# Optimization experiments

Hardware: AMD Instinct MI355X
Metric: run time of the kernel (lower is better)

Reference implementation:

```python
import jax, jax.numpy as jnp
import numpy as np

THRESHOLD = 0.02  # matches init threshold
N_POINTS = 4_000_000
N_PLANES = 64


def setup_inputs() -> dict:
    key = jax.random.key(0)
    k1, k2, k3 = jax.random.split(key, 3)
    points = jax.random.uniform(k1, (N_POINTS, 3), dtype=jnp.float32)
    normals = jax.random.normal(k2, (N_PLANES, 3), dtype=jnp.float32)
    normals = normals / jnp.linalg.norm(normals, axis=1, keepdims=True)
    # anchor each plane at a random point inside the cube so it intersects the cloud
    anchors = jax.random.uniform(k3, (N_PLANES, 3), dtype=jnp.float32)
    distances = jnp.sum(normals * anchors, axis=1)
    return {"points": points, "normals": normals, "distances": distances}


def reference(points, normals, distances):
    """Sequential per-plane SVD refinement + masked projection (faithful to torch loop).

    Plane fits (mask, centroid, covariance) use the ORIGINAL points, as in the
    source; only the projection is applied cumulatively to the running state.
    """
    dtype = points.dtype
    jitter = jnp.diag(jnp.asarray([1.0, 2.0, 3.0], dtype))  # keeps eigh well-posed for invalid planes

    def step(proj, plane):
        n, d = plane
        # inlier mask on original points (data-dependent in torch; here a weight vector)
        m = (jnp.abs(points @ n - d) < THRESHOLD).astype(dtype)  # (N,)
        cnt = jnp.sum(m)
        validf = (cnt >= 3.0).astype(dtype)
        centroid = jnp.sum(m[:, None] * points, axis=0) / jnp.maximum(cnt, 1.0)  # (3,)
        xc = (points - centroid) * m[:, None]  # masked centered points (N,3)
        cov = xc.T @ xc  # (3,3), m is 0/1 so single weighting == mask-select
        cov = cov + (1.0 - validf) * jitter
        # smallest-eigenvalue eigenvector of symmetric cov == torch V[:, 2] (up to sign)
        _, V = jnp.linalg.eigh(cov)
        rn = V[:, 0]
        rn = jnp.where(jnp.dot(rn, n) < 0.0, -rn, rn)  # align with coarse normal
        rd = jnp.dot(centroid, rn)
        # project only masked points of the running state onto refined plane
        delta = (proj @ rn - rd)[:, None] * rn[None, :]  # (N,3)
        proj = proj - (validf * m)[:, None] * delta
        return proj, None

    proj, _ = jax.lax.scan(step, points, (normals, distances))
    return proj
```

## Files before the change

kernel.cpp:

```cpp
#include <hip/hip_runtime.h>
#include <math.h>

#define N_POINTS 4000000
#define N_PLANES 64
#define THRESH   0.02f
#define NVALS    (N_PLANES*10)
#define PPT      16
#define NPAIR    (PPT/2)
#define BLKPTS   (PPT*64)
#define G1       2048
#define ITEMS    2
#define NPB      (G1*ITEMS)
#define NPAD     (NPB*BLKPTS - N_POINTS)
#define FULL_PB  (N_POINTS/BLKPTS)
#define SEG_R    16
#define RTHR     256

typedef float v2f __attribute__((ext_vector_type(2)));

__device__ __forceinline__ v2f pk_fma(v2f a, v2f b, v2f c) {
    v2f d; asm("v_pk_fma_f32 %0, %1, %2, %3" : "=v"(d) : "v"(a), "v"(b), "v"(c)); return d;
}
__device__ __forceinline__ v2f pk_fma_n0(v2f a, v2f b, v2f c) {
    v2f d; asm("v_pk_fma_f32 %0, %1, %2, %3 neg_lo:[1,0,0] neg_hi:[1,0,0]"
               : "=v"(d) : "v"(a), "v"(b), "v"(c)); return d;
}
__device__ __forceinline__ v2f pk_mul(v2f a, v2f b) {
    v2f d; asm("v_pk_mul_f32 %0, %1, %2" : "=v"(d) : "v"(a), "v"(b)); return d;
}
__device__ __forceinline__ v2f pk_mul_clamp(v2f a, v2f b) {
    v2f d; asm("v_pk_mul_f32 %0, %1, %2 clamp" : "=v"(d) : "v"(a), "v"(b)); return d;
}
__device__ __forceinline__ void pk_adda(v2f& acc, v2f a) {
    asm("v_pk_add_f32 %0, %1, %0" : "+v"(acc) : "v"(a));
}
__device__ __forceinline__ void pk_fmaa(v2f& acc, v2f a, v2f b) {
    asm("v_pk_fma_f32 %0, %1, %2, %0" : "+v"(acc) : "v"(a), "v"(b));
}
__device__ __forceinline__ float bperm(int addr, float v) {
    return __uint_as_float(__builtin_amdgcn_ds_bpermute(addr, __float_as_uint(v)));
}

__global__ __launch_bounds__(RTHR, 4)
void reduce_kernel(const float* __restrict__ pts,
                   const float* __restrict__ nrm,
                   const float* __restrict__ dst,
                   float* __restrict__ partials)
{
    const int lane = threadIdx.x & 63;
    const int wid  = threadIdx.x >> 6;

    __shared__ float part[RTHR/64][NVALS];

    const int rotaddr = ((lane + 1) & 63) << 2;

    const v2f TH2N2 = { -(THRESH*THRESH), -(THRESH*THRESH) };
    const v2f NBIG2 = { -1e20f, -1e20f };

    int q = (lane + SEG_R * wid) & 63;
    float pnx = nrm[q*3+0], pny = nrm[q*3+1], pnz = nrm[q*3+2], pnd = -dst[q];

    float tot[10];
#pragma unroll
    for (int i = 0; i < 10; ++i) tot[i] = 0.f;

    v2f PX2[NPAIR], PY2[NPAIR], PZ2[NPAIR];

    for (int it = 0; it < ITEMS; ++it) {
        const int pb = blockIdx.x * ITEMS + it;
        const float* P0 = pts + ((size_t)pb * BLKPTS + lane) * 3;

        if (pb < FULL_PB) {
#pragma unroll
            for (int v = 0; v < NPAIR; ++v) {
                PX2[v] = (v2f){ P0[(2*v)*192+0], P0[(2*v+1)*192+0] };
                PY2[v] = (v2f){ P0[(2*v)*192+1], P0[(2*v+1)*192+1] };
                PZ2[v] = (v2f){ P0[(2*v)*192+2], P0[(2*v+1)*192+2] };
            }
        } else if (pb == FULL_PB) {
#pragma unroll
            for (int v = 0; v < NPAIR; ++v) {
                if (v < 2) {
                    PX2[v] = (v2f){ P0[(2*v)*192+0], P0[(2*v+1)*192+0] };
                    PY2[v] = (v2f){ P0[(2*v)*192+1], P0[(2*v+1)*192+1] };
                    PZ2[v] = (v2f){ P0[(2*v)*192+2], P0[(2*v+1)*192+2] };
                } else {
                    PX2[v] = (v2f){0.f,0.f}; PY2[v] = (v2f){0.f,0.f}; PZ2[v] = (v2f){0.f,0.f};
                }
            }
        } else {
#pragma unroll
            for (int v = 0; v < NPAIR; ++v) {
                PX2[v] = (v2f){0.f,0.f}; PY2[v] = (v2f){0.f,0.f}; PZ2[v] = (v2f){0.f,0.f};
            }
        }

#pragma unroll 1
        for (int r = 0; r < SEG_R; ++r) {
            const v2f nx2 = {pnx,pnx}, ny2 = {pny,pny}, nz2 = {pnz,pnz}, nd2 = {pnd,pnd};
            const int qn = (q + 1) & 63;
            const float fnx = nrm[qn*3+0];
            const float fny = nrm[qn*3+1];
            const float fnz = nrm[qn*3+2];
            const float fnd = -dst[qn];

            v2f b0,b1,b2,b3,b4,b5,b6,b7,b8,b9;
            {
                const v2f t2  = pk_fma(PX2[0], nx2, pk_fma(PY2[0], ny2, pk_fma(PZ2[0], nz2, nd2)));
                const v2f d2  = pk_fma(t2, t2, TH2N2);
                const v2f fm2 = pk_mul_clamp(d2, NBIG2);
                const v2f tx2 = pk_mul(PX2[0], fm2);
                const v2f ty2 = pk_mul(PY2[0], fm2);
                const v2f tz2 = pk_mul(PZ2[0], fm2);
                b0 = fm2; b1 = tx2; b2 = ty2; b3 = tz2;
                b4 = pk_mul(tx2, PX2[0]); b5 = pk_mul(tx2, PY2[0]); b6 = pk_mul(tx2, PZ2[0]);
                b7 = pk_mul(ty2, PY2[0]); b8 = pk_mul(ty2, PZ2[0]); b9 = pk_mul(tz2, PZ2[0]);
            }
#pragma unroll
            for (int v = 1; v < NPAIR; ++v) {
                const v2f t2  = pk_fma(PX2[v], nx2, pk_fma(PY2[v], ny2, pk_fma(PZ2[v], nz2, nd2)));
                const v2f d2  = pk_fma(t2, t2, TH2N2);
                const v2f fm2 = pk_mul_clamp(d2, NBIG2);
                const v2f tx2 = pk_mul(PX2[v], fm2);
                const v2f ty2 = pk_mul(PY2[v], fm2);
                const v2f tz2 = pk_mul(PZ2[v], fm2);
                pk_adda(b0, fm2);
                pk_adda(b1, tx2); pk_adda(b2, ty2); pk_adda(b3, tz2);
                pk_fmaa(b4, tx2, PX2[v]); pk_fmaa(b5, tx2, PY2[v]); pk_fmaa(b6, tx2, PZ2[v]);
                pk_fmaa(b7, ty2, PY2[v]); pk_fmaa(b8, ty2, PZ2[v]); pk_fmaa(b9, tz2, PZ2[v]);
            }

            tot[0] += b0.x + b0.y; tot[1] += b1.x + b1.y; tot[2] += b2.x + b2.y;
            tot[3] += b3.x + b3.y; tot[4] += b4.x + b4.y; tot[5] += b5.x + b5.y;
            tot[6] += b6.x + b6.y; tot[7] += b7.x + b7.y; tot[8] += b8.x + b8.y;
            tot[9] += b9.x + b9.y;
#pragma unroll
            for (int i = 0; i < 10; ++i) tot[i] = bperm(rotaddr, tot[i]);

            pnx = fnx; pny = fny; pnz = fnz; pnd = fnd; q = qn;
        }
    }

    {
        const int wp = (lane + SEG_R * (wid + ITEMS)) & 63;
        float* rr = &part[wid][wp * 10];
#pragma unroll
        for (int i = 0; i < 10; ++i) rr[i] = tot[i];
    }
    __syncthreads();
    for (int v = threadIdx.x; v < NVALS; v += RTHR) {
        float sum = 0.f;
#pragma unroll
        for (int ww = 0; ww < RTHR/64; ++ww) sum += part[ww][v];
        partials[(long long)blockIdx.x * NVALS + v] = sum;
    }
}

__global__ __launch_bounds__(256)
void finalize_kernel(const float* __restrict__ partials, int nb,
                     const float* __restrict__ nrm,
                     const float* __restrict__ dst,
                     float* __restrict__ params)
{
    const int p    = blockIdx.x;
    const int lane = threadIdx.x & 63;
    const int wid  = threadIdx.x >> 6;

    double s[10];
#pragma unroll
    for (int q = 0; q < 10; ++q) s[q] = 0.0;

    for (int b = threadIdx.x; b < nb; b += 256) {
        const float* row = partials + (long long)b * NVALS + p * 10;
#pragma unroll
        for (int q = 0; q < 10; ++q) s[q] += (double)row[q];
    }

#pragma unroll
    for (int off = 32; off; off >>= 1)
#pragma unroll
        for (int q = 0; q < 10; ++q) s[q] += __shfl_xor(s[q], off);

    __shared__ double wsum[4][10];
    if (lane == 0) {
#pragma unroll
        for (int q = 0; q < 10; ++q) wsum[wid][q] = s[q];
    }
    __syncthreads();
    if (threadIdx.x != 0) return;

    double acc[10];
#pragma unroll
    for (int q = 0; q < 10; ++q)
        acc[q] = wsum[0][q] + wsum[1][q] + wsum[2][q] + wsum[3][q];

    double cnt = acc[0];
    if (fmaf(dst[p], dst[p], -(THRESH*THRESH)) < 0.0f) cnt -= (double)NPAD;

    const double sx = acc[1], sy = acc[2], sz = acc[3];
    const double den = fmax(cnt, 1.0);
    const double cx = sx / den, cy = sy / den, cz = sz / den;

    double C[3][3];
    C[0][0] = acc[4] - 2.0*cx*sx + cnt*cx*cx;
    C[0][1] = acc[5] - cx*sy - cy*sx + cnt*cx*cy;
    C[0][2] = acc[6] - cx*sz - cz*sx + cnt*cx*cz;
    C[1][1] = acc[7] - 2.0*cy*sy + cnt*cy*cy;
    C[1][2] = acc[8] - cy*sz - cz*sy + cnt*cy*cz;
    C[2][2] = acc[9] - 2.0*cz*sz + cnt*cz*cz;
    C[1][0] = C[0][1]; C[2][0] = C[0][2]; C[2][1] = C[1][2];

    const double valid = (cnt >= 3.0) ? 1.0 : 0.0;
    C[0][0] += (1.0 - valid) * 1.0;
    C[1][1] += (1.0 - valid) * 2.0;
    C[2][2] += (1.0 - valid) * 3.0;

    double V[3][3] = {{1,0,0},{0,1,0},{0,0,1}};
    for (int sweep = 0; sweep < 15; ++sweep) {
#pragma unroll
        for (int k = 0; k < 3; ++k) {
            const int pp = (k == 2) ? 1 : 0;
            const int qq = (k == 0) ? 1 : 2;
            const int rr = 3 - pp - qq;
            const double apq = C[pp][qq];
            if (fabs(apq) < 1e-300) continue;
            const double theta = (C[qq][qq] - C[pp][pp]) / (2.0 * apq);
            const double t = copysign(1.0, theta) / (fabs(theta) + sqrt(theta*theta + 1.0));
            const double c = 1.0 / sqrt(t*t + 1.0);
            const double ss = t * c;
            const double app = C[pp][pp], aqq = C[qq][qq];
            const double arp = C[rr][pp], arq = C[rr][qq];
            C[pp][pp] = app - t * apq;
            C[qq][qq] = aqq + t * apq;
            C[pp][qq] = 0.0; C[qq][pp] = 0.0;
            const double nrp = c*arp - ss*arq;
            const double nrq = ss*arp + c*arq;
            C[rr][pp] = nrp; C[pp][rr] = nrp;
            C[rr][qq] = nrq; C[qq][rr] = nrq;
#pragma unroll
            for (int i = 0; i < 3; ++i) {
                const double vip = V[i][pp], viq = V[i][qq];
                V[i][pp] = c*vip - ss*viq;
                V[i][qq] = ss*vip + c*viq;
            }
        }
    }

    int idx = 0;
    if (C[1][1] < C[idx][idx]) idx = 1;
    if (C[2][2] < C[idx][idx]) idx = 2;
    double rx = V[0][idx], ry = V[1][idx], rz = V[2][idx];
    const double inv = 1.0 / sqrt(rx*rx + ry*ry + rz*rz);
    rx *= inv; ry *= inv; rz *= inv;

    const double nxd = (double)nrm[p*3+0];
    const double nyd = (double)nrm[p*3+1];
    const double nzd = (double)nrm[p*3+2];
    if (rx*nxd + ry*nyd + rz*nzd < 0.0) { rx = -rx; ry = -ry; rz = -rz; }
    const double rd = cx*rx + cy*ry + cz*rz;

    const float vldf = (float)valid;
    params[p*8+0] = nrm[p*3+0];
    params[p*8+1] = nrm[p*3+1];
    params[p*8+2] = nrm[p*3+2];
    params[p*8+3] = -dst[p];
    params[p*8+4] = vldf * (float)rx;
    params[p*8+5] = vldf * (float)ry;
    params[p*8+6] = vldf * (float)rz;
    params[p*8+7] = -(vldf * (float)rd);
}

#define PPTH 8
#define PQ   (N_POINTS / PPTH)

__global__ __launch_bounds__(256)
void project_kernel(const float* __restrict__ pts,
                    const float* __restrict__ params,
                    float* __restrict__ out)
{
    const int tid = blockIdx.x * 256 + threadIdx.x;
    if (tid >= PQ) return;

    const v2f TH2N2 = { -(THRESH*THRESH), -(THRESH*THRESH) };
    const v2f NBIG2 = { -1e20f, -1e20f };

    v2f ox2[4], oy2[4], oz2[4], qx2[4], qy2[4], qz2[4];
#pragma unroll
    for (int k = 0; k < 4; ++k) {
        const long long i0 = (long long)tid + (long long)(2*k)   * PQ;
        const long long i1 = (long long)tid + (long long)(2*k+1) * PQ;
        ox2[k] = (v2f){ pts[i0*3+0], pts[i1*3+0] };
        oy2[k] = (v2f){ pts[i0*3+1], pts[i1*3+1] };
        oz2[k] = (v2f){ pts[i0*3+2], pts[i1*3+2] };
        qx2[k] = ox2[k]; qy2[k] = oy2[k]; qz2[k] = oz2[k];
    }

#pragma unroll 2
    for (int p = 0; p < N_PLANES; ++p) {
        const float nx  = params[p*8+0];
        const float ny  = params[p*8+1];
        const float nz  = params[p*8+2];
        const float md  = params[p*8+3];
        const float rvx = params[p*8+4];
        const float rvy = params[p*8+5];
        const float rvz = params[p*8+6];
        const float mrd = params[p*8+7];
        const v2f nx2  = (v2f){nx,nx},   ny2  = (v2f){ny,ny},   nz2 = (v2f){nz,nz};
        const v2f md2  = (v2f){md,md},   mrd2 = (v2f){mrd,mrd};
        const v2f rvx2 = (v2f){rvx,rvx}, rvy2 = (v2f){rvy,rvy}, rvz2 = (v2f){rvz,rvz};

#pragma unroll
        for (int k = 0; k < 4; ++k) {
            const v2f t0  = pk_fma(ox2[k], nx2, pk_fma(oy2[k], ny2, pk_fma(oz2[k], nz2, md2)));
            const v2f d2  = pk_fma(t0, t0, TH2N2);
            const v2f fm2 = pk_mul_clamp(d2, NBIG2);
            const v2f tt  = pk_fma(qx2[k], rvx2, pk_fma(qy2[k], rvy2, pk_fma(qz2[k], rvz2, mrd2)));
            const v2f ft  = pk_mul(tt, fm2);
            qx2[k] = pk_fma_n0(ft, rvx2, qx2[k]);
            qy2[k] = pk_fma_n0(ft, rvy2, qy2[k]);
            qz2[k] = pk_fma_n0(ft, rvz2, qz2[k]);
        }
    }

#pragma unroll
    for (int k = 0; k < 4; ++k) {
        const long long i0 = (long long)tid + (long long)(2*k)   * PQ;
        const long long i1 = (long long)tid + (long long)(2*k+1) * PQ;
        out[i0*3+0] = qx2[k].x; out[i0*3+1] = qy2[k].x; out[i0*3+2] = qz2[k].x;
        out[i1*3+0] = qx2[k].y; out[i1*3+1] = qy2[k].y; out[i1*3+2] = qz2[k].y;
    }
}

extern "C" void kernel_launch(void* const* d_in, const int* in_sizes, int n_in,
                              void* d_out, int out_size, void* d_ws, size_t ws_size,
                              hipStream_t stream)
{
    const float* pts = (const float*)d_in[0];
    const float* nrm = (const float*)d_in[1];
    const float* dst = (const float*)d_in[2];
    float* out = (float*)d_out;

    float* partials = (float*)d_ws;
    size_t poff = ((size_t)G1 * NVALS * sizeof(float) + 255) & ~(size_t)255;
    float* params = (float*)((char*)d_ws + poff);

    hipLaunchKernelGGL(reduce_kernel, dim3(G1), dim3(RTHR), 0, stream,
                       pts, nrm, dst, partials);
    hipLaunchKernelGGL(finalize_kernel, dim3(N_PLANES), dim3(256), 0, stream,
                       partials, G1, nrm, dst, params);
    hipLaunchKernelGGL(project_kernel, dim3((PQ + 255) / 256), dim3(256), 0, stream,
                       pts, params, out);
}
```

Measured before the change: 172.2 us.

## Pack two planes per lane with op_sel to drop per-round horizontal adds

The reduction kernel now evaluates two different planes in the lo and hi halves of each packed register. It uses op_sel modifiers to broadcast one point component against both planes. Packed accumulators hold per-plane sums directly, which removes the per-round horizontal add of lo/hi halves into scalar totals. Rotation rounds are halved and the grid/items split is retuned to keep plane coverage. The final write uses a store-then-accumulate pattern into shared memory, which relies on intra-wave ordering.

```diff
diff --git a/kernel.cpp b/kernel.cpp
--- a/kernel.cpp
+++ b/kernel.cpp
@@ -8,12 +8,12 @@
 #define PPT      16
 #define NPAIR    (PPT/2)
 #define BLKPTS   (PPT*64)
-#define G1       2048
-#define ITEMS    2
+#define G1       1024
+#define ITEMS    4
 #define NPB      (G1*ITEMS)
 #define NPAD     (NPB*BLKPTS - N_POINTS)
 #define FULL_PB  (N_POINTS/BLKPTS)
-#define SEG_R    16
+#define SEG_R    8
 #define RTHR     256
 
 typedef float v2f __attribute__((ext_vector_type(2)));
@@ -34,8 +34,29 @@
 __device__ __forceinline__ void pk_adda(v2f& acc, v2f a) {
     asm("v_pk_add_f32 %0, %1, %0" : "+v"(acc) : "v"(a));
 }
-__device__ __forceinline__ void pk_fmaa(v2f& acc, v2f a, v2f b) {
-    asm("v_pk_fma_f32 %0, %1, %2, %0" : "+v"(acc) : "v"(a), "v"(b));
+__device__ __forceinline__ v2f pk_fma_lo(v2f a, v2f b, v2f c) {
+    v2f d; asm("v_pk_fma_f32 %0, %1, %2, %3 op_sel:[0,0,0] op_sel_hi:[0,1,1]"
+               : "=v"(d) : "v"(a), "v"(b), "v"(c)); return d;
+}
+__device__ __forceinline__ v2f pk_fma_hi(v2f a, v2f b, v2f c) {
+    v2f d; asm("v_pk_fma_f32 %0, %1, %2, %3 op_sel:[1,0,0] op_sel_hi:[1,1,1]"
+               : "=v"(d) : "v"(a), "v"(b), "v"(c)); return d;
+}
+__device__ __forceinline__ void pk_fmaa_lo(v2f& acc, v2f a, v2f b) {
+    asm("v_pk_fma_f32 %0, %1, %2, %0 op_sel:[0,0,0] op_sel_hi:[0,1,1]"
+        : "+v"(acc) : "v"(a), "v"(b));
+}
+__device__ __forceinline__ void pk_fmaa_hi(v2f& acc, v2f a, v2f b) {
+    asm("v_pk_fma_f32 %0, %1, %2, %0 op_sel:[1,0,0] op_sel_hi:[1,1,1]"
+        : "+v"(acc) : "v"(a), "v"(b));
+}
+__device__ __forceinline__ v2f pk_mul_lo(v2f a, v2f b) {
+    v2f d; asm("v_pk_mul_f32 %0, %1, %2 op_sel:[0,0] op_sel_hi:[0,1]"
+               : "=v"(d) : "v"(a), "v"(b)); return d;
+}
+__device__ __forceinline__ v2f pk_mul_hi(v2f a, v2f b) {
+    v2f d; asm("v_pk_mul_f32 %0, %1, %2 op_sel:[1,0] op_sel_hi:[1,1]"
+               : "=v"(d) : "v"(a), "v"(b)); return d;
 }
 __device__ __forceinline__ float bperm(int addr, float v) {
     return __uint_as_float(__builtin_amdgcn_ds_bpermute(addr, __float_as_uint(v)));
@@ -57,12 +78,18 @@
     const v2f TH2N2 = { -(THRESH*THRESH), -(THRESH*THRESH) };
     const v2f NBIG2 = { -1e20f, -1e20f };
 
-    int q = (lane + SEG_R * wid) & 63;
-    float pnx = nrm[q*3+0], pny = nrm[q*3+1], pnz = nrm[q*3+2], pnd = -dst[q];
-
-    float tot[10];
-#pragma unroll
-    for (int i = 0; i < 10; ++i) tot[i] = 0.f;
+    int qA = (lane + SEG_R * wid) & 63;
+    v2f nxpk, nypk, nzpk, ndpk;
+    {
+        const int qB = (qA + 32) & 63;
+        nxpk = (v2f){ nrm[qA*3+0], nrm[qB*3+0] };
+        nypk = (v2f){ nrm[qA*3+1], nrm[qB*3+1] };
+        nzpk = (v2f){ nrm[qA*3+2], nrm[qB*3+2] };
+        ndpk = (v2f){ -dst[qA],    -dst[qB]    };
+    }
+
+    v2f T0={0,0},T1={0,0},T2={0,0},T3={0,0},T4={0,0};
+    v2f T5={0,0},T6={0,0},T7={0,0},T8={0,0},T9={0,0};
 
     v2f PX2[NPAIR], PY2[NPAIR], PZ2[NPAIR];
 
@@ -97,55 +124,73 @@
 
 #pragma unroll 1
         for (int r = 0; r < SEG_R; ++r) {
-            const v2f nx2 = {pnx,pnx}, ny2 = {pny,pny}, nz2 = {pnz,pnz}, nd2 = {pnd,pnd};
-            const int qn = (q + 1) & 63;
-            const float fnx = nrm[qn*3+0];
-            const float fny = nrm[qn*3+1];
-            const float fnz = nrm[qn*3+2];
-            const float fnd = -dst[qn];
-
-            v2f b0,b1,b2,b3,b4,b5,b6,b7,b8,b9;
-            {
-                const v2f t2  = pk_fma(PX2[0], nx2, pk_fma(PY2[0], ny2, pk_fma(PZ2[0], nz2, nd2)));
-                const v2f d2  = pk_fma(t2, t2, TH2N2);
-                const v2f fm2 = pk_mul_clamp(d2, NBIG2);
-                const v2f tx2 = pk_mul(PX2[0], fm2);
-                const v2f ty2 = pk_mul(PY2[0], fm2);
-                const v2f tz2 = pk_mul(PZ2[0], fm2);
-                b0 = fm2; b1 = tx2; b2 = ty2; b3 = tz2;
-                b4 = pk_mul(tx2, PX2[0]); b5 = pk_mul(tx2, PY2[0]); b6 = pk_mul(tx2, PZ2[0]);
-                b7 = pk_mul(ty2, PY2[0]); b8 = pk_mul(ty2, PZ2[0]); b9 = pk_mul(tz2, PZ2[0]);
-            }
-#pragma unroll
-            for (int v = 1; v < NPAIR; ++v) {
-                const v2f t2  = pk_fma(PX2[v], nx2, pk_fma(PY2[v], ny2, pk_fma(PZ2[v], nz2, nd2)));
-                const v2f d2  = pk_fma(t2, t2, TH2N2);
-                const v2f fm2 = pk_mul_clamp(d2, NBIG2);
-                const v2f tx2 = pk_mul(PX2[v], fm2);
-                const v2f ty2 = pk_mul(PY2[v], fm2);
-                const v2f tz2 = pk_mul(PZ2[v], fm2);
-                pk_adda(b0, fm2);
-                pk_adda(b1, tx2); pk_adda(b2, ty2); pk_adda(b3, tz2);
-                pk_fmaa(b4, tx2, PX2[v]); pk_fmaa(b5, tx2, PY2[v]); pk_fmaa(b6, tx2, PZ2[v]);
-                pk_fmaa(b7, ty2, PY2[v]); pk_fmaa(b8, ty2, PZ2[v]); pk_fmaa(b9, tz2, PZ2[v]);
-            }
-
-            tot[0] += b0.x + b0.y; tot[1] += b1.x + b1.y; tot[2] += b2.x + b2.y;
-            tot[3] += b3.x + b3.y; tot[4] += b4.x + b4.y; tot[5] += b5.x + b5.y;
-            tot[6] += b6.x + b6.y; tot[7] += b7.x + b7.y; tot[8] += b8.x + b8.y;
-            tot[9] += b9.x + b9.y;
-#pragma unroll
-            for (int i = 0; i < 10; ++i) tot[i] = bperm(rotaddr, tot[i]);
-
-            pnx = fnx; pny = fny; pnz = fnz; pnd = fnd; q = qn;
+            const int qn = (qA + 1) & 63;
+            const int qm = (qn + 32) & 63;
+            const float fnxA = nrm[qn*3+0], fnxB = nrm[qm*3+0];
+            const float fnyA = nrm[qn*3+1], fnyB = nrm[qm*3+1];
+            const float fnzA = nrm[qn*3+2], fnzB = nrm[qm*3+2];
+            const float fndA = -dst[qn],    fndB = -dst[qm];
+
+#pragma unroll
+            for (int v = 0; v < NPAIR; ++v) {
+                {
+                    const v2f t2  = pk_fma_lo(PX2[v], nxpk,
+                                    pk_fma_lo(PY2[v], nypk,
+                                    pk_fma_lo(PZ2[v], nzpk, ndpk)));
+                    const v2f d2  = pk_fma(t2, t2, TH2N2);
+                    const v2f fm2 = pk_mul_clamp(d2, NBIG2);
+                    const v2f tx2 = pk_mul_lo(PX2[v], fm2);
+                    const v2f ty2 = pk_mul_lo(PY2[v], fm2);
+                    const v2f tz2 = pk_mul_lo(PZ2[v], fm2);
+                    pk_adda(T0, fm2);
+                    pk_adda(T1, tx2); pk_adda(T2, ty2); pk_adda(T3, tz2);
+                    pk_fmaa_lo(T4, PX2[v], tx2); pk_fmaa_lo(T5, PY2[v], tx2);
+                    pk_fmaa_lo(T6, PZ2[v], tx2); pk_fmaa_lo(T7, PY2[v], ty2);
+                    pk_fmaa_lo(T8, PZ2[v], ty2); pk_fmaa_lo(T9, PZ2[v], tz2);
+                }
+                {
+                    const v2f t2  = pk_fma_hi(PX2[v], nxpk,
+                                    pk_fma_hi(PY2[v], nypk,
+                                    pk_fma_hi(PZ2[v], nzpk, ndpk)));
+                    const v2f d2  = pk_fma(t2, t2, TH2N2);
+                    const v2f fm2 = pk_mul_clamp(d2, NBIG2);
+                    const v2f tx2 = pk_mul_hi(PX2[v], fm2);
+                    const v2f ty2 = pk_mul_hi(PY2[v], fm2);
+                    const v2f tz2 = pk_mul_hi(PZ2[v], fm2);
+                    pk_adda(T0, fm2);
+                    pk_adda(T1, tx2); pk_adda(T2, ty2); pk_adda(T3, tz2);
+                    pk_fmaa_hi(T4, PX2[v], tx2); pk_fmaa_hi(T5, PY2[v], tx2);
+                    pk_fmaa_hi(T6, PZ2[v], tx2); pk_fmaa_hi(T7, PY2[v], ty2);
+                    pk_fmaa_hi(T8, PZ2[v], ty2); pk_fmaa_hi(T9, PZ2[v], tz2);
+                }
+            }
+
+            T0.x = bperm(rotaddr, T0.x); T0.y = bperm(rotaddr, T0.y);
+            T1.x = bperm(rotaddr, T1.x); T1.y = bperm(rotaddr, T1.y);
+            T2.x = bperm(rotaddr, T2.x); T2.y = bperm(rotaddr, T2.y);
+            T3.x = bperm(rotaddr, T3.x); T3.y = bperm(rotaddr, T3.y);
+            T4.x = bperm(rotaddr, T4.x); T4.y = bperm(rotaddr, T4.y);
+            T5.x = bperm(rotaddr, T5.x); T5.y = bperm(rotaddr, T5.y);
+            T6.x = bperm(rotaddr, T6.x); T6.y = bperm(rotaddr, T6.y);
+            T7.x = bperm(rotaddr, T7.x); T7.y = bperm(rotaddr, T7.y);
+            T8.x = bperm(rotaddr, T8.x); T8.y = bperm(rotaddr, T8.y);
+            T9.x = bperm(rotaddr, T9.x); T9.y = bperm(rotaddr, T9.y);
+
+            nxpk = (v2f){fnxA, fnxB}; nypk = (v2f){fnyA, fnyB};
+            nzpk = (v2f){fnzA, fnzB}; ndpk = (v2f){fndA, fndB};
+            qA = qn;
         }
     }
 
     {
-        const int wp = (lane + SEG_R * (wid + ITEMS)) & 63;
-        float* rr = &part[wid][wp * 10];
-#pragma unroll
-        for (int i = 0; i < 10; ++i) rr[i] = tot[i];
+        const int wpA = (lane + SEG_R * wid + SEG_R * ITEMS) & 63;
+        const int wpB = (wpA + 32) & 63;
+        float* rA = &part[wid][wpA * 10];
+        rA[0]=T0.x; rA[1]=T1.x; rA[2]=T2.x; rA[3]=T3.x; rA[4]=T4.x;
+        rA[5]=T5.x; rA[6]=T6.x; rA[7]=T7.x; rA[8]=T8.x; rA[9]=T9.x;
+        float* rB = &part[wid][wpB * 10];
+        rB[0]+=T0.y; rB[1]+=T1.y; rB[2]+=T2.y; rB[3]+=T3.y; rB[4]+=T4.y;
+        rB[5]+=T5.y; rB[6]+=T6.y; rB[7]+=T7.y; rB[8]+=T8.y; rB[9]+=T9.y;
     }
     __syncthreads();
     for (int v = threadIdx.x; v < NVALS; v += RTHR) {
```

New measurement: 171.1 us. Within noise of the previous version (-0.7%).
